# Performance work log

Hardware: AMD Instinct MI355X
Metric: run time of the kernel (lower is better)

The kernel has to match this reference:

```python
import jax, jax.numpy as jnp
import numpy as np

B, N = 4096, 8192
RETURN_W, SHARPE_W, CONC_W, CONF_W, BENT_W, AUX_W = 1.0, 0.1, 0.01, 0.1, 0.01, 0.1
RETURN_TEMP = 20.0
NEG = -1e30
EPS = 1e-8


def setup_inputs() -> dict:
    key = jax.random.key(0)
    ks = jax.random.split(key, 6)
    portfolio_returns = jax.random.normal(ks[0], (B,), dtype=jnp.float32) * 0.01
    weights = jax.random.uniform(ks[1], (B, N), dtype=jnp.float32)
    confidence = jax.random.uniform(ks[2], (B, N), dtype=jnp.float32)
    actual_returns = jax.random.normal(ks[3], (B, N), dtype=jnp.float32) * 0.02
    masks = (jax.random.uniform(ks[4], (B, N)) > 0.1).astype(jnp.float32)
    scores = jax.random.normal(ks[5], (B, N), dtype=jnp.float32)
    return {
        "portfolio_returns": portfolio_returns,
        "weights": weights,
        "confidence": confidence,
        "actual_returns": actual_returns,
        "masks": masks,
        "scores": scores,
    }


def _ranking_loss(scores, returns, masks):
    # Vectorized ListNet loss: masked softmax over valid stocks per sample.
    valid = masks > 0  # (B, N) bool
    n_valid = valid.sum(axis=-1)  # (B,)
    target = jax.nn.softmax(jnp.where(valid, returns * RETURN_TEMP, NEG), axis=-1)
    log_dist = jax.nn.log_softmax(jnp.where(valid, scores, NEG), axis=-1)
    per_sample = -(target * jnp.where(valid, log_dist, 0.0)).sum(axis=-1)
    per_sample = per_sample / jnp.maximum(n_valid, 1).astype(per_sample.dtype)
    sample_ok = n_valid >= 2  # (B,) samples with >=2 valid stocks
    num_ok = sample_ok.sum()
    total = jnp.where(sample_ok, per_sample, 0.0).sum()
    return jnp.where(num_ok > 0, total / jnp.maximum(num_ok, 1), 0.0)


def reference(portfolio_returns, weights, confidence, actual_returns, masks, scores):
    # return maximization
    mean_return = portfolio_returns.mean()
    return_loss = -mean_return
    # sharpe (batch_size > 1; torch .std() uses ddof=1)
    return_std = jnp.std(portfolio_returns, ddof=1)
    sharpe_loss = jnp.clip(-mean_return / (return_std + 0.01), -10.0, 10.0)
    # concentration (weight entropy)
    concentration_loss = -(weights * jnp.log(weights + EPS)).sum(axis=-1).mean()
    # confidence loss
    selected_conf = (weights * confidence * masks).sum(axis=-1)
    total_weight = (weights * masks).sum(axis=-1) + EPS
    per_sample_conf = selected_conf / total_weight
    conf_targets = jax.nn.sigmoid(portfolio_returns * 50.0)
    confidence_loss = jnp.mean((per_sample_conf - conf_targets) ** 2)
    # batch entropy (stocks never valid contribute exactly 0, so no index-filter needed)
    normalized_weights = weights / (weights.sum(axis=-1, keepdims=True) + EPS)
    avg_sel = (normalized_weights * masks).mean(axis=0)  # (N,)
    avg_sel = avg_sel / (avg_sel.sum() + EPS)
    batch_entropy = -(avg_sel * jnp.log(avg_sel + EPS)).sum()
    batch_entropy_loss = -batch_entropy
    # auxiliary ranking loss
    auxiliary_loss = _ranking_loss(scores, actual_returns, masks)
    total_loss = (
        RETURN_W * return_loss
        + SHARPE_W * sharpe_loss
        + CONC_W * concentration_loss
        + CONF_W * confidence_loss
        + BENT_W * batch_entropy_loss
        + AUX_W * auxiliary_loss
    )
    return total_loss
```

## Files before the change

kernel.cpp:

```cpp
#include <hip/hip_runtime.h>
#include <math.h>

#define BB 4096
#define NN 8192
#define EPSF 1e-8f

typedef float f32x4 __attribute__((ext_vector_type(4)));

#define SCAL 4096
#define CS   8192
#define PP   16384

__global__ void init_ws(float* __restrict__ ws) {
    int i = blockIdx.x * blockDim.x + threadIdx.x;
    if (i < 12288) ws[SCAL + i] = 0.f;
}

template<int MODE>
__global__ __launch_bounds__(512) void main_k(
    const float* __restrict__ pr, const float* __restrict__ w,
    const float* __restrict__ cf, const float* __restrict__ ar,
    const float* __restrict__ mk, const float* __restrict__ sc,
    float* ws)
{
    extern __shared__ f32x4 wlds[];
    __shared__ float rpark[8][4];
    __shared__ float park[4][8][8];

    const int t = threadIdx.x;
    const int wave = t >> 6, lane = t & 63;
    const int rowBase = blockIdx.x * 4;

    const size_t rbase = (size_t)rowBase * (NN / 4);
    const f32x4* w4 = (const f32x4*)w;
    const f32x4* m4 = (const f32x4*)mk;
    const f32x4* c4 = (const f32x4*)cf;
    const f32x4* a4 = (const f32x4*)ar;
    const f32x4* s4 = (const f32x4*)sc;

    float rs0, rs1, rs2, rs3;
    {
        float rsv[4];
#pragma unroll
        for (int rr = 0; rr < 4; ++rr) {
            float acc = 0.f;
#pragma unroll
            for (int j = 0; j < 4; ++j) {
                const int idx = rr * 2048 + j * 512 + t;
                const f32x4 v = __builtin_nontemporal_load(w4 + rbase + idx);
                wlds[idx] = v;
                acc += (v.x + v.y) + (v.z + v.w);
            }
            rsv[rr] = acc;
        }
        rs0 = rsv[0]; rs1 = rsv[1]; rs2 = rsv[2]; rs3 = rsv[3];
    }
#pragma unroll
    for (int off = 32; off; off >>= 1) {
        rs0 += __shfl_xor(rs0, off);
        rs1 += __shfl_xor(rs1, off);
        rs2 += __shfl_xor(rs2, off);
        rs3 += __shfl_xor(rs3, off);
    }
    if (lane == 0) {
        rpark[wave][0] = rs0; rpark[wave][1] = rs1;
        rpark[wave][2] = rs2; rpark[wave][3] = rs3;
    }
    __syncthreads();

    float inv[4];
#pragma unroll
    for (int r = 0; r < 4; ++r) {
        float acc = 0.f;
#pragma unroll
        for (int k = 0; k < 8; ++k) acc += rpark[k][r];
        inv[r] = 1.f / (acc + EPSF);
    }

    float csum[16];
#pragma unroll
    for (int j = 0; j < 16; ++j) csum[j] = 0.f;

#define PROC(WK, MKV, CK, RK, SK, IDX) {                          \
        const float wk = (WK), mval = (MKV);                      \
        conc = fmaf(wk, __logf(wk + EPSF), conc);                 \
        const float wmk = wk * mval;                              \
        tw += wmk; scf = fmaf(wmk, (CK), scf);                    \
        nv += mval;                                               \
        const float er = __expf((RK) * 20.f) * mval;              \
        Zr += er; A = fmaf(er, (SK), A);                          \
        Zs = fmaf(__expf((SK)), mval, Zs);                        \
        csum[IDX] = fmaf(wmk, invr, csum[IDX]); }

#pragma unroll
    for (int rr = 0; rr < 4; ++rr) {
        const size_t base = rbase + (size_t)rr * (NN / 4) + t;
        const float invr = inv[rr];
        float conc = 0.f, scf = 0.f, tw = 0.f, nv = 0.f;
        float Zr = 0.f, A = 0.f, Zs = 0.f;
#pragma unroll
        for (int j = 0; j < 4; ++j) {
            const f32x4 wv = wlds[rr * 2048 + j * 512 + t];
            const f32x4 mv = __builtin_nontemporal_load(m4 + base + j * 512);
            const f32x4 cv = __builtin_nontemporal_load(c4 + base + j * 512);
            const f32x4 rv = __builtin_nontemporal_load(a4 + base + j * 512);
            const f32x4 sv = __builtin_nontemporal_load(s4 + base + j * 512);
            PROC(wv.x, mv.x, cv.x, rv.x, sv.x, j * 4 + 0)
            PROC(wv.y, mv.y, cv.y, rv.y, sv.y, j * 4 + 1)
            PROC(wv.z, mv.z, cv.z, rv.z, sv.z, j * 4 + 2)
            PROC(wv.w, mv.w, cv.w, rv.w, sv.w, j * 4 + 3)
        }
#pragma unroll
        for (int off = 32; off; off >>= 1) {
            conc += __shfl_xor(conc, off);
            scf  += __shfl_xor(scf, off);
            tw   += __shfl_xor(tw, off);
            nv   += __shfl_xor(nv, off);
            Zr   += __shfl_xor(Zr, off);
            A    += __shfl_xor(A, off);
            Zs   += __shfl_xor(Zs, off);
        }
        if (lane == 0) {
            float* p = park[rr][wave];
            p[0] = conc; p[1] = scf; p[2] = tw; p[3] = nv;
            p[4] = Zr;   p[5] = A;   p[6] = Zs;
        }
    }
#undef PROC

    if (MODE == 1) {
        f32x4* dst = (f32x4*)(ws + PP) + (size_t)blockIdx.x * (NN / 4);
#pragma unroll
        for (int j = 0; j < 4; ++j) {
            f32x4 v;
            v.x = csum[j * 4 + 0]; v.y = csum[j * 4 + 1];
            v.z = csum[j * 4 + 2]; v.w = csum[j * 4 + 3];
            __builtin_nontemporal_store(v, dst + t + j * 512);
        }
    } else {
#pragma unroll
        for (int j = 0; j < 4; ++j) {
            const int f4 = t + j * 512;
            atomicAdd(&ws[CS + 4 * f4 + 0], csum[j * 4 + 0]);
            atomicAdd(&ws[CS + 4 * f4 + 1], csum[j * 4 + 1]);
            atomicAdd(&ws[CS + 4 * f4 + 2], csum[j * 4 + 2]);
            atomicAdd(&ws[CS + 4 * f4 + 3], csum[j * 4 + 3]);
        }
    }

    __syncthreads();

    if (t < 64) {
        float c0 = 0.f, c1 = 0.f, c2 = 0.f, c3 = 0.f;
        if (lane < 4) {
            float CO = 0, SC = 0, TW = 0, NV = 0, ZR = 0, AA = 0, ZS = 0;
#pragma unroll
            for (int k = 0; k < 8; ++k) {
                const float* p = park[lane][k];
                CO += p[0]; SC += p[1]; TW += p[2]; NV += p[3];
                ZR += p[4]; AA += p[5]; ZS += p[6];
            }
            c0 = CO;
            const float psc = SC / (TW + EPSF);
            const float ct = 1.f / (1.f + __expf(-50.f * pr[rowBase + lane]));
            const float d = psc - ct;
            c1 = d * d;
            if (NV >= 2.f) {
                c2 = (__logf(ZS) - AA / ZR) / NV;
                c3 = 1.f;
            }
        }
        c0 += __shfl_xor(c0, 1); c0 += __shfl_xor(c0, 2);
        c1 += __shfl_xor(c1, 1); c1 += __shfl_xor(c1, 2);
        c2 += __shfl_xor(c2, 1); c2 += __shfl_xor(c2, 2);
        c3 += __shfl_xor(c3, 1); c3 += __shfl_xor(c3, 2);
        if (lane == 0) {
            atomicAdd(&ws[SCAL + 0], c0);
            atomicAdd(&ws[SCAL + 1], c1);
            atomicAdd(&ws[SCAL + 2], c2);
            atomicAdd(&ws[SCAL + 3], c3);
        }
    }
}

__global__ __launch_bounds__(256) void colreduce_k(const float* __restrict__ src,
                                                   float* __restrict__ ws) {
    const int c = blockIdx.x * 256 + threadIdx.x;
    const int k0 = blockIdx.y * 128;
    float s = 0.f;
    for (int k = 0; k < 128; ++k) s += src[(size_t)(k0 + k) * NN + c];
    atomicAdd(&ws[CS + c], s);
}

__device__ __forceinline__ float block_sum_1024(float v) {
    __shared__ float scm[16];
#pragma unroll
    for (int off = 32; off; off >>= 1) v += __shfl_xor(v, off);
    if ((threadIdx.x & 63) == 0) scm[threadIdx.x >> 6] = v;
    __syncthreads();
    if (threadIdx.x == 0) {
        float a = 0.f;
        for (int k = 0; k < 16; ++k) a += scm[k];
        scm[0] = a;
    }
    __syncthreads();
    float r = scm[0];
    __syncthreads();
    return r;
}

__global__ __launch_bounds__(1024) void finalize(
    const float* __restrict__ pr, const float* __restrict__ ws,
    float* __restrict__ out)
{
    const int t = threadIdx.x;

    float s = 0.f, ssq = 0.f;
    for (int i = t; i < BB; i += 1024) { float v = pr[i]; s += v; ssq = fmaf(v, v, ssq); }
    float Tc = 0.f;
    for (int i = t; i < NN; i += 1024) Tc += ws[CS + i];

    float S  = block_sum_1024(s);
    float SS = block_sum_1024(ssq);
    float T  = block_sum_1024(Tc);

    const float mean = S / (float)BB;
    const float denom = T / (float)BB + EPSF;

    float ent = 0.f;
    for (int i = t; i < NN; i += 1024) {
        float a = ws[CS + i] / (float)BB;
        float na = a / denom;
        ent = fmaf(na, __logf(na + EPSF), ent);
    }
    float ENT = block_sum_1024(ent);

    if (t == 0) {
        float var = (SS - (float)BB * mean * mean) / (float)(BB - 1);
        float sd = sqrtf(fmaxf(var, 0.f));
        float sharpe = -mean / (sd + 0.01f);
        sharpe = fminf(fmaxf(sharpe, -10.f), 10.f);
        float conc_loss = -ws[SCAL + 0] / (float)BB;
        float conf_loss =  ws[SCAL + 1] / (float)BB;
        float nok = ws[SCAL + 3];
        float aux = (nok > 0.f) ? ws[SCAL + 2] / fmaxf(nok, 1.f) : 0.f;
        out[0] = 1.0f * (-mean)
               + 0.1f * sharpe
               + 0.01f * conc_loss
               + 0.1f * conf_loss
               + 0.01f * ENT
               + 0.1f * aux;
    }
}

extern "C" void kernel_launch(void* const* d_in, const int* in_sizes, int n_in,
                              void* d_out, int out_size, void* d_ws, size_t ws_size,
                              hipStream_t stream) {
    const float* pr = (const float*)d_in[0];
    const float* w  = (const float*)d_in[1];
    const float* cf = (const float*)d_in[2];
    const float* ar = (const float*)d_in[3];
    const float* mk = (const float*)d_in[4];
    const float* sc = (const float*)d_in[5];
    float* ws = (float*)d_ws;
    float* out = (float*)d_out;

    const size_t needBytes = ((size_t)PP + (size_t)1024 * NN) * sizeof(float);
    const bool partial = (ws_size >= needBytes);
    const size_t ldsBytes = 4 * (NN / 4) * sizeof(f32x4);

    init_ws<<<48, 256, 0, stream>>>(ws);
    if (partial) {
        main_k<1><<<1024, 512, ldsBytes, stream>>>(pr, w, cf, ar, mk, sc, ws);
        colreduce_k<<<dim3(32, 8), 256, 0, stream>>>(ws + PP, ws);
    } else {
        main_k<0><<<1024, 512, ldsBytes, stream>>>(pr, w, cf, ar, mk, sc, ws);
    }
    finalize<<<1, 1024, 0, stream>>>(pr, ws, out);
}
```

Before: 159.6 us.

## Halve rows per block, store column partials as bf16, drop init and atomics

```diff
diff --git a/kernel.cpp b/kernel.cpp
--- a/kernel.cpp
+++ b/kernel.cpp
@@ -6,10 +6,18 @@
 #define EPSF 1e-8f
 
 typedef float f32x4 __attribute__((ext_vector_type(4)));
-
+typedef unsigned short u16x4 __attribute__((ext_vector_type(4)));
+
+#define ST2  8192
+#define PPF  73728
 #define SCAL 4096
 #define CS   8192
-#define PP   16384
+
+__device__ __forceinline__ unsigned short f2bf(float f) {
+    union { float f; unsigned u; } v; v.f = f;
+    unsigned u = v.u + 0x7FFF + ((v.u >> 16) & 1);
+    return (unsigned short)(u >> 16);
+}
 
 __global__ void init_ws(float* __restrict__ ws) {
     int i = blockIdx.x * blockDim.x + threadIdx.x;
@@ -24,12 +32,12 @@
     float* ws)
 {
     extern __shared__ f32x4 wlds[];
-    __shared__ float rpark[8][4];
-    __shared__ float park[4][8][8];
+    __shared__ float rpark[8][2];
+    __shared__ float park[2][8][8];
 
     const int t = threadIdx.x;
     const int wave = t >> 6, lane = t & 63;
-    const int rowBase = blockIdx.x * 4;
+    const int rowBase = blockIdx.x * 2;
 
     const size_t rbase = (size_t)rowBase * (NN / 4);
     const f32x4* w4 = (const f32x4*)w;
@@ -38,11 +46,11 @@
     const f32x4* a4 = (const f32x4*)ar;
     const f32x4* s4 = (const f32x4*)sc;
 
-    float rs0, rs1, rs2, rs3;
+    float rs0, rs1;
     {
-        float rsv[4];
-#pragma unroll
-        for (int rr = 0; rr < 4; ++rr) {
+        float rsv[2];
+#pragma unroll
+        for (int rr = 0; rr < 2; ++rr) {
             float acc = 0.f;
 #pragma unroll
             for (int j = 0; j < 4; ++j) {
@@ -53,24 +61,19 @@
             }
             rsv[rr] = acc;
         }
-        rs0 = rsv[0]; rs1 = rsv[1]; rs2 = rsv[2]; rs3 = rsv[3];
+        rs0 = rsv[0]; rs1 = rsv[1];
     }
 #pragma unroll
     for (int off = 32; off; off >>= 1) {
         rs0 += __shfl_xor(rs0, off);
         rs1 += __shfl_xor(rs1, off);
-        rs2 += __shfl_xor(rs2, off);
-        rs3 += __shfl_xor(rs3, off);
-    }
-    if (lane == 0) {
-        rpark[wave][0] = rs0; rpark[wave][1] = rs1;
-        rpark[wave][2] = rs2; rpark[wave][3] = rs3;
-    }
-    __syncthreads();
-
-    float inv[4];
-#pragma unroll
-    for (int r = 0; r < 4; ++r) {
+    }
+    if (lane == 0) { rpark[wave][0] = rs0; rpark[wave][1] = rs1; }
+    __syncthreads();
+
+    float inv[2];
+#pragma unroll
+    for (int r = 0; r < 2; ++r) {
         float acc = 0.f;
 #pragma unroll
         for (int k = 0; k < 8; ++k) acc += rpark[k][r];
@@ -93,7 +96,7 @@
         csum[IDX] = fmaf(wmk, invr, csum[IDX]); }
 
 #pragma unroll
-    for (int rr = 0; rr < 4; ++rr) {
+    for (int rr = 0; rr < 2; ++rr) {
         const size_t base = rbase + (size_t)rr * (NN / 4) + t;
         const float invr = inv[rr];
         float conc = 0.f, scf = 0.f, tw = 0.f, nv = 0.f;
@@ -129,13 +132,13 @@
 #undef PROC
 
     if (MODE == 1) {
-        f32x4* dst = (f32x4*)(ws + PP) + (size_t)blockIdx.x * (NN / 4);
+        unsigned short* bfrow = (unsigned short*)(ws + PPF) + (size_t)blockIdx.x * NN;
 #pragma unroll
         for (int j = 0; j < 4; ++j) {
-            f32x4 v;
-            v.x = csum[j * 4 + 0]; v.y = csum[j * 4 + 1];
-            v.z = csum[j * 4 + 2]; v.w = csum[j * 4 + 3];
-            __builtin_nontemporal_store(v, dst + t + j * 512);
+            u16x4 v;
+            v.x = f2bf(csum[j * 4 + 0]); v.y = f2bf(csum[j * 4 + 1]);
+            v.z = f2bf(csum[j * 4 + 2]); v.w = f2bf(csum[j * 4 + 3]);
+            __builtin_nontemporal_store(v, (u16x4*)bfrow + t + j * 512);
         }
     } else {
 #pragma unroll
@@ -152,7 +155,7 @@
 
     if (t < 64) {
         float c0 = 0.f, c1 = 0.f, c2 = 0.f, c3 = 0.f;
-        if (lane < 4) {
+        if (lane < 2) {
             float CO = 0, SC = 0, TW = 0, NV = 0, ZR = 0, AA = 0, ZS = 0;
 #pragma unroll
             for (int k = 0; k < 8; ++k) {
@@ -170,26 +173,40 @@
                 c3 = 1.f;
             }
         }
-        c0 += __shfl_xor(c0, 1); c0 += __shfl_xor(c0, 2);
-        c1 += __shfl_xor(c1, 1); c1 += __shfl_xor(c1, 2);
-        c2 += __shfl_xor(c2, 1); c2 += __shfl_xor(c2, 2);
-        c3 += __shfl_xor(c3, 1); c3 += __shfl_xor(c3, 2);
+        c0 += __shfl_xor(c0, 1);
+        c1 += __shfl_xor(c1, 1);
+        c2 += __shfl_xor(c2, 1);
+        c3 += __shfl_xor(c3, 1);
         if (lane == 0) {
-            atomicAdd(&ws[SCAL + 0], c0);
-            atomicAdd(&ws[SCAL + 1], c1);
-            atomicAdd(&ws[SCAL + 2], c2);
-            atomicAdd(&ws[SCAL + 3], c3);
-        }
-    }
-}
-
-__global__ __launch_bounds__(256) void colreduce_k(const float* __restrict__ src,
-                                                   float* __restrict__ ws) {
-    const int c = blockIdx.x * 256 + threadIdx.x;
-    const int k0 = blockIdx.y * 128;
-    float s = 0.f;
-    for (int k = 0; k < 128; ++k) s += src[(size_t)(k0 + k) * NN + c];
-    atomicAdd(&ws[CS + c], s);
+            if (MODE == 1) {
+                float* dst = ws + (size_t)blockIdx.x * 4;
+                dst[0] = c0; dst[1] = c1; dst[2] = c2; dst[3] = c3;
+            } else {
+                atomicAdd(&ws[SCAL + 0], c0);
+                atomicAdd(&ws[SCAL + 1], c1);
+                atomicAdd(&ws[SCAL + 2], c2);
+                atomicAdd(&ws[SCAL + 3], c3);
+            }
+        }
+    }
+}
+
+__global__ __launch_bounds__(128) void colreduce_k(const unsigned short* __restrict__ src,
+                                                   float* __restrict__ st2) {
+    const int col4 = blockIdx.x * 128 + threadIdx.x;
+    const int k0 = blockIdx.y * 256;
+    const u16x4* s4 = (const u16x4*)src;
+    float a0 = 0.f, a1 = 0.f, a2 = 0.f, a3 = 0.f;
+    for (int k = 0; k < 256; ++k) {
+        const u16x4 v = s4[(size_t)(k0 + k) * (NN / 4) + col4];
+        union { unsigned u; float f; } b;
+        b.u = (unsigned)v.x << 16; a0 += b.f;
+        b.u = (unsigned)v.y << 16; a1 += b.f;
+        b.u = (unsigned)v.z << 16; a2 += b.f;
+        b.u = (unsigned)v.w << 16; a3 += b.f;
+    }
+    f32x4 o; o.x = a0; o.y = a1; o.z = a2; o.w = a3;
+    *((f32x4*)(st2 + (size_t)blockIdx.y * NN) + col4) = o;
 }
 
 __device__ __forceinline__ float block_sum_1024(float v) {
@@ -209,27 +226,57 @@
     return r;
 }
 
+template<int MODE>
 __global__ __launch_bounds__(1024) void finalize(
     const float* __restrict__ pr, const float* __restrict__ ws,
     float* __restrict__ out)
 {
+    __shared__ float colLDS[NN];
     const int t = threadIdx.x;
 
     float s = 0.f, ssq = 0.f;
     for (int i = t; i < BB; i += 1024) { float v = pr[i]; s += v; ssq = fmaf(v, v, ssq); }
+
+    float p0 = 0.f, p1 = 0.f, p2 = 0.f, p3 = 0.f;
+    if (MODE == 1) {
+        for (int b = t; b < 2048; b += 1024) {
+            p0 += ws[b * 4 + 0]; p1 += ws[b * 4 + 1];
+            p2 += ws[b * 4 + 2]; p3 += ws[b * 4 + 3];
+        }
+    }
+
     float Tc = 0.f;
-    for (int i = t; i < NN; i += 1024) Tc += ws[CS + i];
+    for (int i = t; i < NN; i += 1024) {
+        float cs;
+        if (MODE == 1) {
+            cs = 0.f;
+#pragma unroll
+            for (int k = 0; k < 8; ++k) cs += ws[ST2 + k * NN + i];
+        } else {
+            cs = ws[CS + i];
+        }
+        colLDS[i] = cs;
+        Tc += cs;
+    }
 
     float S  = block_sum_1024(s);
     float SS = block_sum_1024(ssq);
     float T  = block_sum_1024(Tc);
+    float C0, C1, C2, C3;
+    if (MODE == 1) {
+        C0 = block_sum_1024(p0); C1 = block_sum_1024(p1);
+        C2 = block_sum_1024(p2); C3 = block_sum_1024(p3);
+    } else {
+        C0 = ws[SCAL + 0]; C1 = ws[SCAL + 1];
+        C2 = ws[SCAL + 2]; C3 = ws[SCAL + 3];
+    }
 
     const float mean = S / (float)BB;
     const float denom = T / (float)BB + EPSF;
 
     float ent = 0.f;
     for (int i = t; i < NN; i += 1024) {
-        float a = ws[CS + i] / (float)BB;
+        float a = colLDS[i] / (float)BB;
         float na = a / denom;
         ent = fmaf(na, __logf(na + EPSF), ent);
     }
@@ -240,10 +287,9 @@
         float sd = sqrtf(fmaxf(var, 0.f));
         float sharpe = -mean / (sd + 0.01f);
         sharpe = fminf(fmaxf(sharpe, -10.f), 10.f);
-        float conc_loss = -ws[SCAL + 0] / (float)BB;
-        float conf_loss =  ws[SCAL + 1] / (float)BB;
-        float nok = ws[SCAL + 3];
-        float aux = (nok > 0.f) ? ws[SCAL + 2] / fmaxf(nok, 1.f) : 0.f;
+        float conc_loss = -C0 / (float)BB;
+        float conf_loss =  C1 / (float)BB;
+        float aux = (C3 > 0.f) ? C2 / fmaxf(C3, 1.f) : 0.f;
         out[0] = 1.0f * (-mean)
                + 0.1f * sharpe
                + 0.01f * conc_loss
@@ -265,16 +311,17 @@
     float* ws = (float*)d_ws;
     float* out = (float*)d_out;
 
-    const size_t needBytes = ((size_t)PP + (size_t)1024 * NN) * sizeof(float);
-    const bool partial = (ws_size >= needBytes);
-    const size_t ldsBytes = 4 * (NN / 4) * sizeof(f32x4);
-
-    init_ws<<<48, 256, 0, stream>>>(ws);
-    if (partial) {
-        main_k<1><<<1024, 512, ldsBytes, stream>>>(pr, w, cf, ar, mk, sc, ws);
-        colreduce_k<<<dim3(32, 8), 256, 0, stream>>>(ws + PP, ws);
+    const size_t ldsBytes = 2 * (NN / 4) * sizeof(f32x4);
+    const size_t bfNeed = (size_t)PPF * 4 + (size_t)2048 * NN * 2;
+
+    if (ws_size >= bfNeed) {
+        main_k<1><<<2048, 512, ldsBytes, stream>>>(pr, w, cf, ar, mk, sc, ws);
+        colreduce_k<<<dim3(16, 8), 128, 0, stream>>>(
+            (const unsigned short*)(ws + PPF), ws + ST2);
+        finalize<1><<<1, 1024, 0, stream>>>(pr, ws, out);
     } else {
-        main_k<0><<<1024, 512, ldsBytes, stream>>>(pr, w, cf, ar, mk, sc, ws);
-    }
-    finalize<<<1, 1024, 0, stream>>>(pr, ws, out);
-}
+        init_ws<<<48, 256, 0, stream>>>(ws);
+        main_k<0><<<2048, 512, ldsBytes, stream>>>(pr, w, cf, ar, mk, sc, ws);
+        finalize<0><<<1, 1024, 0, stream>>>(pr, ws, out);
+    }
+}
```

After: 151.3 us. 1.05x faster.
